# Optimization experiments

Measured on AMD Instinct MI355X. Metric: run time of the kernel, lower is better.

The kernel has to match this reference:

```python
import jax, jax.numpy as jnp
import numpy as np

ALPHA = 0.2       # leak rate
NOISE_STD = 0.05  # noise_std

B, T, I, H, O = 128, 1024, 64, 512, 10


def setup_inputs() -> dict:
    key = jax.random.key(0)
    k0, k1, k2, k3, k4 = jax.random.split(key, 5)
    inp = jax.random.normal(k0, (B, T, I), dtype=jnp.float32)
    noise = jax.random.normal(k1, (B, T, H), dtype=jnp.float32)
    # parameters, initialized as in FullRankRNN.__init__
    wi = jax.random.normal(k2, (I, H), dtype=jnp.float32)                      # wi ~ N(0,1)
    si = jnp.ones((I,), dtype=jnp.float32)                                     # input scaling
    wrec = jax.random.normal(k3, (H, H), dtype=jnp.float32) * (1.0 / np.sqrt(H))  # rho/sqrt(H), rho=1
    wo = jax.random.normal(k4, (H, O), dtype=jnp.float32) * (5.0 / H)          # std = 5/hidden
    so = jnp.ones((O,), dtype=jnp.float32)                                     # output scaling
    h0 = jnp.zeros((H,), dtype=jnp.float32)
    return {"input": inp, "noise": noise, "wi": wi, "si": si,
            "wrec": wrec, "wo": wo, "so": so, "h0": h0}


def reference(input, noise, wi, si, wrec, wo, so, h0):
    # proxy parameters: wi_full = (wi.T * si).T = wi * si[:,None]; wo_full = wo * so
    wi_full = wi * si[:, None]          # [I, H]
    wo_full = wo * so                   # [H, O] (so broadcasts over output dim)
    h_init = jnp.broadcast_to(h0, (input.shape[0], h0.shape[0]))  # [B, H]

    def step(h, xs):
        x_t, n_t = xs                   # [B, I], [B, H]
        r = jax.nn.relu(h)
        h_new = h + ALPHA * (-h + x_t @ wi_full + r @ wrec.T) + NOISE_STD * n_t
        out_t = jax.nn.relu(h_new) @ wo_full   # [B, O]
        return h_new, out_t

    xs = (jnp.swapaxes(input, 0, 1), jnp.swapaxes(noise, 0, 1))  # time-major
    _, outs = jax.lax.scan(step, h_init, xs)                     # [T, B, O]
    return jnp.swapaxes(outs, 0, 1)                              # [B, T, O]
```

## Files before the change

kernel.cpp:

```cpp
#include <hip/hip_runtime.h>

typedef _Float16 h2 __attribute__((ext_vector_type(2)));
typedef unsigned int uint;
typedef unsigned short ushort;

#define ALPHA 0.2f
#define NSTD  0.05f
#define BB 128
#define TT 1024
#define II 64
#define HH 512
#define OO 10

#define WS_NEED (512 * 12 * 16)

__device__ __forceinline__ float fdot2f(h2 a, h2 b, float c) {
#if __has_builtin(__builtin_amdgcn_fdot2)
    return __builtin_amdgcn_fdot2(a, b, c, false);
#else
    return c + (float)a.x * (float)b.x + (float)a.y * (float)b.y;
#endif
}
__device__ __forceinline__ h2 mkh2(float a, float b) { h2 v; v.x = (_Float16)a; v.y = (_Float16)b; return v; }
__device__ __forceinline__ h2 bch2(uint u) { return __builtin_bit_cast(h2, u); }
__device__ __forceinline__ uint bcu(h2 v) { return __builtin_bit_cast(uint, v); }

#define AGPR_WRITE(dst, src) asm volatile("v_accvgpr_write_b32 %0, %1" : "=a"(dst) : "v"(src))
#define AGPR_READ(dst, src)  asm volatile("v_accvgpr_read_b32 %0, %1" : "=v"(dst) : "a"(src))

template<int CTRL>
__device__ __forceinline__ float dppadd(float v) {
    int i = __builtin_bit_cast(int, v);
    int m = __builtin_amdgcn_update_dpp(0, i, CTRL, 0xF, 0xF, true);
    return v + __builtin_bit_cast(float, m);
}
__device__ __forceinline__ float red64(float v) {
    v = dppadd<0xB1>(v);
    v = dppadd<0x4E>(v);
    v = dppadd<0x124>(v);
    v = dppadd<0x128>(v);
    v = dppadd<0x142>(v);
    v = dppadd<0x143>(v);
    return v;
}

__global__ __launch_bounds__(512) void pack_kernel(
    const float* __restrict__ wrec, const float* __restrict__ wi,
    const float* __restrict__ si, uint4* __restrict__ ws)
{
    const int tid = threadIdx.x;
    const int l = tid & 63, g = tid >> 6;
    uint4* wsp = ws + tid * 12;
#pragma unroll
    for (int r = 0; r < 2; ++r) {
        uint v[8];
#pragma unroll
        for (int c = 0; c < 8; ++c) {
            const float* wr = wrec + (size_t)(c * 64 + l) * HH + g * 64 + 60 + 2 * r;
            v[c] = bcu(mkh2(wr[0], wr[1]));
        }
        wsp[r * 2 + 0] = make_uint4(v[0], v[1], v[2], v[3]);
        wsp[r * 2 + 1] = make_uint4(v[4], v[5], v[6], v[7]);
    }
#pragma unroll
    for (int r = 2; r < 6; ++r) {
        const int k0 = g * 8 + 2 * (r - 2);
        const float sa = si[k0], sb = si[k0 + 1];
        uint v[8];
#pragma unroll
        for (int c = 0; c < 8; ++c) {
            const int j = c * 64 + l;
            v[c] = bcu(mkh2(wi[(size_t)k0 * HH + j] * sa, wi[(size_t)(k0 + 1) * HH + j] * sb));
        }
        wsp[r * 2 + 0] = make_uint4(v[0], v[1], v[2], v[3]);
        wsp[r * 2 + 1] = make_uint4(v[4], v[5], v[6], v[7]);
    }
}

template<bool PACKED>
__global__ __launch_bounds__(512, 2) void rnn_kernel(
    const float* __restrict__ input, const float* __restrict__ noise,
    const float* __restrict__ wi, const float* __restrict__ si,
    const float* __restrict__ wrec, const float* __restrict__ wo,
    const float* __restrict__ so, const float* __restrict__ h0,
    const uint4* __restrict__ wsS, float* __restrict__ out)
{
    __shared__ uint4 ldsw[16 * 512];
    __shared__ float hacc_w[8][HH];
    __shared__ __align__(16) ushort r_shm[8 * 72];
    __shared__ uint  wo2m[OO * 256];
    __shared__ float opart[8][8];

    const int tid = threadIdx.x, l = tid & 63, g = tid >> 6;
    const int b = blockIdx.x;
    const int jown = g * 64 + l;

    uint wa[22][8];
#pragma unroll
    for (int c = 0; c < 8; ++c) {
        const float* wr = wrec + (size_t)(c * 64 + l) * HH + g * 64;
#pragma unroll
        for (int p = 0; p < 22; ++p) {
            uint v = bcu(mkh2(wr[2 * p], wr[2 * p + 1]));
            AGPR_WRITE(wa[p][c], v);
        }
    }
#pragma unroll
    for (int c = 0; c < 8; ++c) {
        const float* wr = wrec + (size_t)(c * 64 + l) * HH + g * 64 + 44;
        uint4 v1, v2;
        v1.x = bcu(mkh2(wr[0], wr[1]));   v1.y = bcu(mkh2(wr[2], wr[3]));
        v1.z = bcu(mkh2(wr[4], wr[5]));   v1.w = bcu(mkh2(wr[6], wr[7]));
        v2.x = bcu(mkh2(wr[8], wr[9]));   v2.y = bcu(mkh2(wr[10], wr[11]));
        v2.z = bcu(mkh2(wr[12], wr[13])); v2.w = bcu(mkh2(wr[14], wr[15]));
        ldsw[(2 * c) * 512 + tid] = v1;
        ldsw[(2 * c + 1) * 512 + tid] = v2;
    }
    float si8[8];
    if (!PACKED) {
#pragma unroll
        for (int e = 0; e < 8; ++e) si8[e] = si[g * 8 + e];
    }
    if (g < 4) {
#pragma unroll
        for (int o = 0; o < OO; ++o) {
            float sA = so[o] * (1.0f / ALPHA);
            wo2m[o * 256 + g * 64 + l] =
                bcu(mkh2(wo[(size_t)(g * 128 + l) * OO + o] * sA,
                         wo[(size_t)(g * 128 + 64 + l) * OO + o] * sA));
        }
    }
    float hreg = h0[jown];
    ((_Float16*)r_shm)[g * 72 + l] = (_Float16)(ALPHA * fmaxf(hreg, 0.f));
    if (g == 0) {
        float x0 = input[(size_t)b * TT * II + l];
        ((_Float16*)r_shm)[(l >> 3) * 72 + 64 + (l & 7)] = (_Float16)(ALPHA * x0);
    }
    __syncthreads();

    const uint4* r4 = ((const uint4*)r_shm) + g * 9;
    const uint4* wsp = wsS + tid * 12;
    int nidx = b * TT * HH + jown;
    const int ob = (g >> 2) * 5, q = g & 3;
    const int pa = (2 * q) * 72 + l, pb = pa + 72;
    float* outp = out + (size_t)b * TT * OO;

    auto out_duty = [&]() {
        h2 rr; rr.x = ((const _Float16*)r_shm)[pa]; rr.y = ((const _Float16*)r_shm)[pb];
        float op0 = fdot2f(rr, bch2(wo2m[(ob + 0) * 256 + q * 64 + l]), 0.f);
        float op1 = fdot2f(rr, bch2(wo2m[(ob + 1) * 256 + q * 64 + l]), 0.f);
        float op2 = fdot2f(rr, bch2(wo2m[(ob + 2) * 256 + q * 64 + l]), 0.f);
        float op3 = fdot2f(rr, bch2(wo2m[(ob + 3) * 256 + q * 64 + l]), 0.f);
        float op4 = fdot2f(rr, bch2(wo2m[(ob + 4) * 256 + q * 64 + l]), 0.f);
        op0 = red64(op0); op1 = red64(op1); op2 = red64(op2);
        op3 = red64(op3); op4 = red64(op4);
        if (l == 63) {
            opart[g][0] = op0; opart[g][1] = op1; opart[g][2] = op2;
            opart[g][3] = op3; opart[g][4] = op4;
        }
    };

    uint4 R0g = r4[0], R1g = r4[1];

#pragma unroll 1
    for (int t = 0; t < TT; ++t) {
        float nval = noise[nidx]; nidx += HH;
        float xnext = 0.f;
        if (g == 0 && t + 1 < TT) xnext = input[(size_t)b * TT * II + (size_t)(t + 1) * II + l];

        out_duty();

        float acc[8] = {0.f, 0.f, 0.f, 0.f, 0.f, 0.f, 0.f, 0.f};

#pragma unroll
        for (int qq = 0; qq < 5; ++qq) {
            uint4 R = (qq == 0) ? R0g : (qq == 1) ? R1g : r4[qq];
            uint rc[4] = {R.x, R.y, R.z, R.w};
#pragma unroll
            for (int pp = 0; pp < 4; ++pp) {
                const h2 rr = bch2(rc[pp]);
                const int p = 4 * qq + pp;
#pragma unroll
                for (int c = 0; c < 8; ++c) {
                    uint wv; AGPR_READ(wv, wa[p][c]);
                    acc[c] = fdot2f(bch2(wv), rr, acc[c]);
                }
            }
        }
        uint4 R5 = r4[5], R6 = r4[6], R7 = r4[7], R8 = r4[8];
        {
            const h2 r20 = bch2(R5.x), r21 = bch2(R5.y);
#pragma unroll
            for (int c = 0; c < 8; ++c) {
                uint w0, w1;
                AGPR_READ(w0, wa[20][c]); AGPR_READ(w1, wa[21][c]);
                acc[c] = fdot2f(bch2(w0), r20, acc[c]);
                acc[c] = fdot2f(bch2(w1), r21, acc[c]);
            }
        }
        {
            const h2 r22 = bch2(R5.z), r23 = bch2(R5.w);
            const h2 r24 = bch2(R6.x), r25 = bch2(R6.y), r26 = bch2(R6.z), r27 = bch2(R6.w);
            const h2 r28 = bch2(R7.x), r29 = bch2(R7.y);
#pragma unroll
            for (int c = 0; c < 8; ++c) {
                uint4 L1 = ldsw[(2 * c) * 512 + tid];
                uint4 L2 = ldsw[(2 * c + 1) * 512 + tid];
                acc[c] = fdot2f(bch2(L1.x), r22, acc[c]);
                acc[c] = fdot2f(bch2(L1.y), r23, acc[c]);
                acc[c] = fdot2f(bch2(L1.z), r24, acc[c]);
                acc[c] = fdot2f(bch2(L1.w), r25, acc[c]);
                acc[c] = fdot2f(bch2(L2.x), r26, acc[c]);
                acc[c] = fdot2f(bch2(L2.y), r27, acc[c]);
                acc[c] = fdot2f(bch2(L2.z), r28, acc[c]);
                acc[c] = fdot2f(bch2(L2.w), r29, acc[c]);
            }
        }
        {
            const h2 r30 = bch2(R7.z), r31 = bch2(R7.w);
            const h2 r32 = bch2(R8.x), r33 = bch2(R8.y), r34 = bch2(R8.z), r35 = bch2(R8.w);
            if (PACKED) {
#pragma unroll
                for (int h = 0; h < 2; ++h) {
                    uint4 S0 = wsp[0 * 2 + h], S1 = wsp[1 * 2 + h], S2 = wsp[2 * 2 + h];
                    uint4 S3 = wsp[3 * 2 + h], S4 = wsp[4 * 2 + h], S5 = wsp[5 * 2 + h];
                    uint s0[4] = {S0.x, S0.y, S0.z, S0.w}; uint s1[4] = {S1.x, S1.y, S1.z, S1.w};
                    uint s2[4] = {S2.x, S2.y, S2.z, S2.w}; uint s3[4] = {S3.x, S3.y, S3.z, S3.w};
                    uint s4[4] = {S4.x, S4.y, S4.z, S4.w}; uint s5[4] = {S5.x, S5.y, S5.z, S5.w};
#pragma unroll
                    for (int cc = 0; cc < 4; ++cc) {
                        const int c = 4 * h + cc;
                        acc[c] = fdot2f(bch2(s0[cc]), r30, acc[c]);
                        acc[c] = fdot2f(bch2(s1[cc]), r31, acc[c]);
                        acc[c] = fdot2f(bch2(s2[cc]), r32, acc[c]);
                        acc[c] = fdot2f(bch2(s3[cc]), r33, acc[c]);
                        acc[c] = fdot2f(bch2(s4[cc]), r34, acc[c]);
                        acc[c] = fdot2f(bch2(s5[cc]), r35, acc[c]);
                    }
                }
            } else {
#pragma unroll
                for (int c = 0; c < 8; ++c) {
                    const int j = c * 64 + l;
                    const float* wr = wrec + (size_t)j * HH + g * 64 + 60;
                    float4 f = *(const float4*)wr;
                    acc[c] = fdot2f(mkh2(f.x, f.y), r30, acc[c]);
                    acc[c] = fdot2f(mkh2(f.z, f.w), r31, acc[c]);
                    float a0 = wi[(size_t)(g * 8 + 0) * HH + j] * si8[0];
                    float a1 = wi[(size_t)(g * 8 + 1) * HH + j] * si8[1];
                    float a2 = wi[(size_t)(g * 8 + 2) * HH + j] * si8[2];
                    float a3 = wi[(size_t)(g * 8 + 3) * HH + j] * si8[3];
                    float a4 = wi[(size_t)(g * 8 + 4) * HH + j] * si8[4];
                    float a5 = wi[(size_t)(g * 8 + 5) * HH + j] * si8[5];
                    float a6 = wi[(size_t)(g * 8 + 6) * HH + j] * si8[6];
                    float a7 = wi[(size_t)(g * 8 + 7) * HH + j] * si8[7];
                    acc[c] = fdot2f(mkh2(a0, a1), r32, acc[c]);
                    acc[c] = fdot2f(mkh2(a2, a3), r33, acc[c]);
                    acc[c] = fdot2f(mkh2(a4, a5), r34, acc[c]);
                    acc[c] = fdot2f(mkh2(a6, a7), r35, acc[c]);
                }
            }
        }
#pragma unroll
        for (int c = 0; c < 8; ++c) hacc_w[g][c * 64 + l] = acc[c];
        __syncthreads();

        if (g == 7 && l < OO && t > 0) {
            float v;
            if (l < 5) v = opart[0][l] + opart[1][l] + opart[2][l] + opart[3][l];
            else { int o = l - 5; v = opart[4][o] + opart[5][o] + opart[6][o] + opart[7][o]; }
            outp[(size_t)(t - 1) * OO + l] = v;
        }
        {
            float s0 = hacc_w[0][jown], s1 = hacc_w[1][jown];
            float s2 = hacc_w[2][jown], s3 = hacc_w[3][jown];
            float s4 = hacc_w[4][jown], s5 = hacc_w[5][jown];
            float s6 = hacc_w[6][jown], s7 = hacc_w[7][jown];
            float s = ((s0 + s1) + (s2 + s3)) + ((s4 + s5) + (s6 + s7));
            hreg = (1.f - ALPHA) * hreg + s + NSTD * nval;
        }
        ((_Float16*)r_shm)[g * 72 + l] = (_Float16)(ALPHA * fmaxf(hreg, 0.f));
        if (g == 0) ((_Float16*)r_shm)[(l >> 3) * 72 + 64 + (l & 7)] = (_Float16)(ALPHA * xnext);
        asm volatile("" ::: "memory");
        R0g = r4[0]; R1g = r4[1];
        __syncthreads();
    }

    out_duty();
    __syncthreads();
    if (g == 7 && l < OO) {
        float v;
        if (l < 5) v = opart[0][l] + opart[1][l] + opart[2][l] + opart[3][l];
        else { int o = l - 5; v = opart[4][o] + opart[5][o] + opart[6][o] + opart[7][o]; }
        outp[(size_t)(TT - 1) * OO + l] = v;
    }
}

extern "C" void kernel_launch(void* const* d_in, const int* in_sizes, int n_in,
                              void* d_out, int out_size, void* d_ws, size_t ws_size,
                              hipStream_t stream) {
    const float* input = (const float*)d_in[0];
    const float* noise = (const float*)d_in[1];
    const float* wi    = (const float*)d_in[2];
    const float* si    = (const float*)d_in[3];
    const float* wrec  = (const float*)d_in[4];
    const float* wo    = (const float*)d_in[5];
    const float* so    = (const float*)d_in[6];
    const float* h0    = (const float*)d_in[7];
    float* out = (float*)d_out;

    if (ws_size >= (size_t)WS_NEED) {
        uint4* ws = (uint4*)d_ws;
        pack_kernel<<<dim3(1), dim3(512), 0, stream>>>(wrec, wi, si, ws);
        rnn_kernel<true><<<dim3(BB), dim3(512), 0, stream>>>(
            input, noise, wi, si, wrec, wo, so, h0, ws, out);
    } else {
        rnn_kernel<false><<<dim3(BB), dim3(512), 0, stream>>>(
            input, noise, wi, si, wrec, wo, so, h0, nullptr, out);
    }
}
```

Baseline: 3.591 ms.

## Batch 16 sequences per block and compute recurrence with MFMA

Replaces the per-sequence fdot2 recurrence with blocks that each process 16 batch rows, computing the recurrent, input and output projections with 16x16x32 f16 MFMA instructions. Most recurrent weights stay in registers as MFMA B-fragments, with the remainder in LDS. Hidden state is kept in accumulator layout, and the relu'd state is double-buffered in LDS so each step needs only one barrier. The grid shrinks to 8 blocks, trading parallelism across CUs for much less serial work per step. The separate pack kernel and workspace path are removed.

```diff
diff --git a/kernel.cpp b/kernel.cpp
--- a/kernel.cpp
+++ b/kernel.cpp
@@ -1,8 +1,8 @@
 #include <hip/hip_runtime.h>
 
-typedef _Float16 h2 __attribute__((ext_vector_type(2)));
-typedef unsigned int uint;
-typedef unsigned short ushort;
+typedef _Float16 f16;
+typedef _Float16 f16x8 __attribute__((ext_vector_type(8)));
+typedef float    f32x4 __attribute__((ext_vector_type(4)));
 
 #define ALPHA 0.2f
 #define NSTD  0.05f
@@ -12,287 +12,219 @@
 #define HH 512
 #define OO 10
 
-#define WS_NEED (512 * 12 * 16)
-
-__device__ __forceinline__ float fdot2f(h2 a, h2 b, float c) {
-#if __has_builtin(__builtin_amdgcn_fdot2)
-    return __builtin_amdgcn_fdot2(a, b, c, false);
-#else
-    return c + (float)a.x * (float)b.x + (float)a.y * (float)b.y;
-#endif
+#define MB   16
+#define NB   (BB / MB)
+#define NAG  13
+#define NLD  3
+#define RSTR 584
+
+__device__ __forceinline__ f32x4 mfma16(f16x8 a, f16x8 b, f32x4 c) {
+    return __builtin_amdgcn_mfma_f32_16x16x32_f16(a, b, c, 0, 0, 0);
 }
-__device__ __forceinline__ h2 mkh2(float a, float b) { h2 v; v.x = (_Float16)a; v.y = (_Float16)b; return v; }
-__device__ __forceinline__ h2 bch2(uint u) { return __builtin_bit_cast(h2, u); }
-__device__ __forceinline__ uint bcu(h2 v) { return __builtin_bit_cast(uint, v); }
-
-#define AGPR_WRITE(dst, src) asm volatile("v_accvgpr_write_b32 %0, %1" : "=a"(dst) : "v"(src))
-#define AGPR_READ(dst, src)  asm volatile("v_accvgpr_read_b32 %0, %1" : "=v"(dst) : "a"(src))
-
-template<int CTRL>
-__device__ __forceinline__ float dppadd(float v) {
-    int i = __builtin_bit_cast(int, v);
-    int m = __builtin_amdgcn_update_dpp(0, i, CTRL, 0xF, 0xF, true);
-    return v + __builtin_bit_cast(float, m);
-}
-__device__ __forceinline__ float red64(float v) {
-    v = dppadd<0xB1>(v);
-    v = dppadd<0x4E>(v);
-    v = dppadd<0x124>(v);
-    v = dppadd<0x128>(v);
-    v = dppadd<0x142>(v);
-    v = dppadd<0x143>(v);
-    return v;
-}
-
-__global__ __launch_bounds__(512) void pack_kernel(
-    const float* __restrict__ wrec, const float* __restrict__ wi,
-    const float* __restrict__ si, uint4* __restrict__ ws)
-{
-    const int tid = threadIdx.x;
-    const int l = tid & 63, g = tid >> 6;
-    uint4* wsp = ws + tid * 12;
-#pragma unroll
-    for (int r = 0; r < 2; ++r) {
-        uint v[8];
-#pragma unroll
-        for (int c = 0; c < 8; ++c) {
-            const float* wr = wrec + (size_t)(c * 64 + l) * HH + g * 64 + 60 + 2 * r;
-            v[c] = bcu(mkh2(wr[0], wr[1]));
-        }
-        wsp[r * 2 + 0] = make_uint4(v[0], v[1], v[2], v[3]);
-        wsp[r * 2 + 1] = make_uint4(v[4], v[5], v[6], v[7]);
-    }
-#pragma unroll
-    for (int r = 2; r < 6; ++r) {
-        const int k0 = g * 8 + 2 * (r - 2);
-        const float sa = si[k0], sb = si[k0 + 1];
-        uint v[8];
-#pragma unroll
-        for (int c = 0; c < 8; ++c) {
-            const int j = c * 64 + l;
-            v[c] = bcu(mkh2(wi[(size_t)k0 * HH + j] * sa, wi[(size_t)(k0 + 1) * HH + j] * sb));
-        }
-        wsp[r * 2 + 0] = make_uint4(v[0], v[1], v[2], v[3]);
-        wsp[r * 2 + 1] = make_uint4(v[4], v[5], v[6], v[7]);
-    }
-}
-
-template<bool PACKED>
+
 __global__ __launch_bounds__(512, 2) void rnn_kernel(
     const float* __restrict__ input, const float* __restrict__ noise,
     const float* __restrict__ wi, const float* __restrict__ si,
     const float* __restrict__ wrec, const float* __restrict__ wo,
     const float* __restrict__ so, const float* __restrict__ h0,
-    const uint4* __restrict__ wsS, float* __restrict__ out)
+    float* __restrict__ out)
 {
-    __shared__ uint4 ldsw[16 * 512];
-    __shared__ float hacc_w[8][HH];
-    __shared__ __align__(16) ushort r_shm[8 * 72];
-    __shared__ uint  wo2m[OO * 256];
-    __shared__ float opart[8][8];
+    __shared__ __align__(16) f16 r_lds[2][MB][RSTR];
+    __shared__ f16x8 wrecL[NLD][32][64];
+    __shared__ f32x4 opart[2][8][64];
 
     const int tid = threadIdx.x, l = tid & 63, g = tid >> 6;
-    const int b = blockIdx.x;
-    const int jown = g * 64 + l;
-
-    uint wa[22][8];
-#pragma unroll
-    for (int c = 0; c < 8; ++c) {
-        const float* wr = wrec + (size_t)(c * 64 + l) * HH + g * 64;
-#pragma unroll
-        for (int p = 0; p < 22; ++p) {
-            uint v = bcu(mkh2(wr[2 * p], wr[2 * p + 1]));
-            AGPR_WRITE(wa[p][c], v);
-        }
-    }
-#pragma unroll
-    for (int c = 0; c < 8; ++c) {
-        const float* wr = wrec + (size_t)(c * 64 + l) * HH + g * 64 + 44;
-        uint4 v1, v2;
-        v1.x = bcu(mkh2(wr[0], wr[1]));   v1.y = bcu(mkh2(wr[2], wr[3]));
-        v1.z = bcu(mkh2(wr[4], wr[5]));   v1.w = bcu(mkh2(wr[6], wr[7]));
-        v2.x = bcu(mkh2(wr[8], wr[9]));   v2.y = bcu(mkh2(wr[10], wr[11]));
-        v2.z = bcu(mkh2(wr[12], wr[13])); v2.w = bcu(mkh2(wr[14], wr[15]));
-        ldsw[(2 * c) * 512 + tid] = v1;
-        ldsw[(2 * c + 1) * 512 + tid] = v2;
-    }
-    float si8[8];
-    if (!PACKED) {
-#pragma unroll
-        for (int e = 0; e < 8; ++e) si8[e] = si[g * 8 + e];
-    }
-    if (g < 4) {
-#pragma unroll
-        for (int o = 0; o < OO; ++o) {
-            float sA = so[o] * (1.0f / ALPHA);
-            wo2m[o * 256 + g * 64 + l] =
-                bcu(mkh2(wo[(size_t)(g * 128 + l) * OO + o] * sA,
-                         wo[(size_t)(g * 128 + 64 + l) * OO + o] * sA));
-        }
-    }
-    float hreg = h0[jown];
-    ((_Float16*)r_shm)[g * 72 + l] = (_Float16)(ALPHA * fmaxf(hreg, 0.f));
-    if (g == 0) {
-        float x0 = input[(size_t)b * TT * II + l];
-        ((_Float16*)r_shm)[(l >> 3) * 72 + 64 + (l & 7)] = (_Float16)(ALPHA * x0);
-    }
+    const int lr = l & 15, lg = l >> 4;
+    const int b0 = blockIdx.x * MB;
+
+    f16x8 bw[NAG][4];
+    f16x8 bwi[2][4];
+    f16x8 bwo[2];
+
+#pragma unroll
+    for (int kt = 0; kt < NAG; ++kt)
+#pragma unroll
+        for (int nt = 0; nt < 4; ++nt) {
+            const float* wp = wrec + (size_t)((4*g + nt)*16 + lr)*HH + kt*32 + lg*8;
+            float4 a0 = *(const float4*)wp;
+            float4 a1 = *(const float4*)(wp + 4);
+            f16x8 v;
+            v[0]=(f16)a0.x; v[1]=(f16)a0.y; v[2]=(f16)a0.z; v[3]=(f16)a0.w;
+            v[4]=(f16)a1.x; v[5]=(f16)a1.y; v[6]=(f16)a1.z; v[7]=(f16)a1.w;
+            bw[kt][nt] = v;
+        }
+#pragma unroll
+    for (int ktL = 0; ktL < NLD; ++ktL)
+#pragma unroll
+        for (int c = 0; c < 4; ++c) {
+            const int nt = c*8 + g;
+            const float* wp = wrec + (size_t)(nt*16 + lr)*HH + (NAG + ktL)*32 + lg*8;
+            float4 a0 = *(const float4*)wp;
+            float4 a1 = *(const float4*)(wp + 4);
+            f16x8 v;
+            v[0]=(f16)a0.x; v[1]=(f16)a0.y; v[2]=(f16)a0.z; v[3]=(f16)a0.w;
+            v[4]=(f16)a1.x; v[5]=(f16)a1.y; v[6]=(f16)a1.z; v[7]=(f16)a1.w;
+            wrecL[ktL][nt][l] = v;
+        }
+#pragma unroll
+    for (int k2 = 0; k2 < 2; ++k2)
+#pragma unroll
+        for (int nt = 0; nt < 4; ++nt) {
+            const int hcol = (4*g + nt)*16 + lr;
+            f16x8 v;
+#pragma unroll
+            for (int jj = 0; jj < 8; ++jj) {
+                const int i = k2*32 + lg*8 + jj;
+                v[jj] = (f16)(wi[(size_t)i*HH + hcol] * si[i]);
+            }
+            bwi[k2][nt] = v;
+        }
+    {
+        const float s = (lr < OO) ? so[lr] * (1.0f/ALPHA) : 0.0f;
+#pragma unroll
+        for (int k2 = 0; k2 < 2; ++k2) {
+            f16x8 v;
+#pragma unroll
+            for (int jj = 0; jj < 8; ++jj) {
+                const int k = (2*g + k2)*32 + lg*8 + jj;
+                v[jj] = (f16)((lr < OO) ? wo[(size_t)k*OO + lr] * s : 0.0f);
+            }
+            bwo[k2] = v;
+        }
+    }
+
+    f32x4 hs[4];
+#pragma unroll
+    for (int nt = 0; nt < 4; ++nt) {
+        const float v = h0[(4*g + nt)*16 + lr];
+        hs[nt] = f32x4{v, v, v, v};
+    }
+
+    const float* nptr[4];
+#pragma unroll
+    for (int rr = 0; rr < 4; ++rr)
+        nptr[rr] = noise + (size_t)(b0 + 4*lg + rr)*TT*HH + 64*g + lr;
+    float nz[4][4];
+#pragma unroll
+    for (int nt = 0; nt < 4; ++nt)
+#pragma unroll
+        for (int rr = 0; rr < 4; ++rr) nz[nt][rr] = nptr[rr][nt*16];
+
+    const int bb = tid >> 5, ii = (tid & 31) * 2;
+    const float* xbase = input + (size_t)(b0 + bb)*TT*II + ii;
+    float2 xv = *(const float2*)xbase;
+
+#pragma unroll
+    for (int nt = 0; nt < 4; ++nt)
+#pragma unroll
+        for (int rr = 0; rr < 4; ++rr)
+            r_lds[0][4*lg + rr][(4*g + nt)*16 + lr] =
+                (f16)(ALPHA * fmaxf(hs[nt][rr], 0.0f));
+    r_lds[0][bb][512 + ii]     = (f16)(ALPHA * xv.x);
+    r_lds[0][bb][512 + ii + 1] = (f16)(ALPHA * xv.y);
+    const float* xq = xbase + II;
+    xv = *(const float2*)xq;  xq += II;
+
     __syncthreads();
 
-    const uint4* r4 = ((const uint4*)r_shm) + g * 9;
-    const uint4* wsp = wsS + tid * 12;
-    int nidx = b * TT * HH + jown;
-    const int ob = (g >> 2) * 5, q = g & 3;
-    const int pa = (2 * q) * 72 + l, pb = pa + 72;
-    float* outp = out + (size_t)b * TT * OO;
-
-    auto out_duty = [&]() {
-        h2 rr; rr.x = ((const _Float16*)r_shm)[pa]; rr.y = ((const _Float16*)r_shm)[pb];
-        float op0 = fdot2f(rr, bch2(wo2m[(ob + 0) * 256 + q * 64 + l]), 0.f);
-        float op1 = fdot2f(rr, bch2(wo2m[(ob + 1) * 256 + q * 64 + l]), 0.f);
-        float op2 = fdot2f(rr, bch2(wo2m[(ob + 2) * 256 + q * 64 + l]), 0.f);
-        float op3 = fdot2f(rr, bch2(wo2m[(ob + 3) * 256 + q * 64 + l]), 0.f);
-        float op4 = fdot2f(rr, bch2(wo2m[(ob + 4) * 256 + q * 64 + l]), 0.f);
-        op0 = red64(op0); op1 = red64(op1); op2 = red64(op2);
-        op3 = red64(op3); op4 = red64(op4);
-        if (l == 63) {
-            opart[g][0] = op0; opart[g][1] = op1; opart[g][2] = op2;
-            opart[g][3] = op3; opart[g][4] = op4;
-        }
-    };
-
-    uint4 R0g = r4[0], R1g = r4[1];
-
+    int cur = 0;
 #pragma unroll 1
     for (int t = 0; t < TT; ++t) {
-        float nval = noise[nidx]; nidx += HH;
-        float xnext = 0.f;
-        if (g == 0 && t + 1 < TT) xnext = input[(size_t)b * TT * II + (size_t)(t + 1) * II + l];
-
-        out_duty();
-
-        float acc[8] = {0.f, 0.f, 0.f, 0.f, 0.f, 0.f, 0.f, 0.f};
-
-#pragma unroll
-        for (int qq = 0; qq < 5; ++qq) {
-            uint4 R = (qq == 0) ? R0g : (qq == 1) ? R1g : r4[qq];
-            uint rc[4] = {R.x, R.y, R.z, R.w};
-#pragma unroll
-            for (int pp = 0; pp < 4; ++pp) {
-                const h2 rr = bch2(rc[pp]);
-                const int p = 4 * qq + pp;
-#pragma unroll
-                for (int c = 0; c < 8; ++c) {
-                    uint wv; AGPR_READ(wv, wa[p][c]);
-                    acc[c] = fdot2f(bch2(wv), rr, acc[c]);
-                }
+        const f16* rb = &r_lds[cur][0][0] + lr*RSTR + lg*8;
+
+#pragma unroll
+        for (int nt = 0; nt < 4; ++nt) {
+            f32x4 a = hs[nt];
+#pragma unroll
+            for (int rr = 0; rr < 4; ++rr)
+                a[rr] = (1.0f - ALPHA)*a[rr] + NSTD*nz[nt][rr];
+            hs[nt] = a;
+        }
+        if (t + 1 < TT) {
+#pragma unroll
+            for (int rr = 0; rr < 4; ++rr) nptr[rr] += HH;
+#pragma unroll
+            for (int nt = 0; nt < 4; ++nt)
+#pragma unroll
+                for (int rr = 0; rr < 4; ++rr) nz[nt][rr] = nptr[rr][nt*16];
+        }
+
+        {
+            const f16x8 aA = *(const f16x8*)(rb + (2*g)*32);
+            const f16x8 aB = *(const f16x8*)(rb + (2*g)*32 + 32);
+            f32x4 oacc = mfma16(aA, bwo[0], f32x4{0.f, 0.f, 0.f, 0.f});
+            oacc = mfma16(aB, bwo[1], oacc);
+            opart[cur][g][l] = oacc;
+        }
+
+#pragma unroll
+        for (int kt = 0; kt < NAG; ++kt) {
+            const f16x8 a = *(const f16x8*)(rb + kt*32);
+#pragma unroll
+            for (int nt = 0; nt < 4; ++nt)
+                hs[nt] = mfma16(a, bw[kt][nt], hs[nt]);
+        }
+#pragma unroll
+        for (int ktL = 0; ktL < NLD; ++ktL) {
+            const f16x8 a = *(const f16x8*)(rb + (NAG + ktL)*32);
+#pragma unroll
+            for (int nt = 0; nt < 4; ++nt)
+                hs[nt] = mfma16(a, wrecL[ktL][4*g + nt][l], hs[nt]);
+        }
+#pragma unroll
+        for (int k2 = 0; k2 < 2; ++k2) {
+            const f16x8 a = *(const f16x8*)(rb + (16 + k2)*32);
+#pragma unroll
+            for (int nt = 0; nt < 4; ++nt)
+                hs[nt] = mfma16(a, bwi[k2][nt], hs[nt]);
+        }
+
+        const int nxt = cur ^ 1;
+#pragma unroll
+        for (int nt = 0; nt < 4; ++nt)
+#pragma unroll
+            for (int rr = 0; rr < 4; ++rr)
+                r_lds[nxt][4*lg + rr][(4*g + nt)*16 + lr] =
+                    (f16)(ALPHA * fmaxf(hs[nt][rr], 0.0f));
+        if (t + 1 < TT) {
+            r_lds[nxt][bb][512 + ii]     = (f16)(ALPHA * xv.x);
+            r_lds[nxt][bb][512 + ii + 1] = (f16)(ALPHA * xv.y);
+            if (t + 2 < TT) { xv = *(const float2*)xq; xq += II; }
+        }
+
+        __syncthreads();
+
+        if (g == 7 && t > 0) {
+            f32x4 s = opart[cur][0][l];
+#pragma unroll
+            for (int w = 1; w < 8; ++w) s += opart[cur][w][l];
+            if (lr < OO) {
+#pragma unroll
+                for (int rr = 0; rr < 4; ++rr)
+                    out[((size_t)(b0 + 4*lg + rr)*TT + (t - 1))*OO + lr] = s[rr];
             }
         }
-        uint4 R5 = r4[5], R6 = r4[6], R7 = r4[7], R8 = r4[8];
-        {
-            const h2 r20 = bch2(R5.x), r21 = bch2(R5.y);
-#pragma unroll
-            for (int c = 0; c < 8; ++c) {
-                uint w0, w1;
-                AGPR_READ(w0, wa[20][c]); AGPR_READ(w1, wa[21][c]);
-                acc[c] = fdot2f(bch2(w0), r20, acc[c]);
-                acc[c] = fdot2f(bch2(w1), r21, acc[c]);
-            }
-        }
-        {
-            const h2 r22 = bch2(R5.z), r23 = bch2(R5.w);
-            const h2 r24 = bch2(R6.x), r25 = bch2(R6.y), r26 = bch2(R6.z), r27 = bch2(R6.w);
-            const h2 r28 = bch2(R7.x), r29 = bch2(R7.y);
-#pragma unroll
-            for (int c = 0; c < 8; ++c) {
-                uint4 L1 = ldsw[(2 * c) * 512 + tid];
-                uint4 L2 = ldsw[(2 * c + 1) * 512 + tid];
-                acc[c] = fdot2f(bch2(L1.x), r22, acc[c]);
-                acc[c] = fdot2f(bch2(L1.y), r23, acc[c]);
-                acc[c] = fdot2f(bch2(L1.z), r24, acc[c]);
-                acc[c] = fdot2f(bch2(L1.w), r25, acc[c]);
-                acc[c] = fdot2f(bch2(L2.x), r26, acc[c]);
-                acc[c] = fdot2f(bch2(L2.y), r27, acc[c]);
-                acc[c] = fdot2f(bch2(L2.z), r28, acc[c]);
-                acc[c] = fdot2f(bch2(L2.w), r29, acc[c]);
-            }
-        }
-        {
-            const h2 r30 = bch2(R7.z), r31 = bch2(R7.w);
-            const h2 r32 = bch2(R8.x), r33 = bch2(R8.y), r34 = bch2(R8.z), r35 = bch2(R8.w);
-            if (PACKED) {
-#pragma unroll
-                for (int h = 0; h < 2; ++h) {
-                    uint4 S0 = wsp[0 * 2 + h], S1 = wsp[1 * 2 + h], S2 = wsp[2 * 2 + h];
-                    uint4 S3 = wsp[3 * 2 + h], S4 = wsp[4 * 2 + h], S5 = wsp[5 * 2 + h];
-                    uint s0[4] = {S0.x, S0.y, S0.z, S0.w}; uint s1[4] = {S1.x, S1.y, S1.z, S1.w};
-                    uint s2[4] = {S2.x, S2.y, S2.z, S2.w}; uint s3[4] = {S3.x, S3.y, S3.z, S3.w};
-                    uint s4[4] = {S4.x, S4.y, S4.z, S4.w}; uint s5[4] = {S5.x, S5.y, S5.z, S5.w};
-#pragma unroll
-                    for (int cc = 0; cc < 4; ++cc) {
-                        const int c = 4 * h + cc;
-                        acc[c] = fdot2f(bch2(s0[cc]), r30, acc[c]);
-                        acc[c] = fdot2f(bch2(s1[cc]), r31, acc[c]);
-                        acc[c] = fdot2f(bch2(s2[cc]), r32, acc[c]);
-                        acc[c] = fdot2f(bch2(s3[cc]), r33, acc[c]);
-                        acc[c] = fdot2f(bch2(s4[cc]), r34, acc[c]);
-                        acc[c] = fdot2f(bch2(s5[cc]), r35, acc[c]);
-                    }
-                }
-            } else {
-#pragma unroll
-                for (int c = 0; c < 8; ++c) {
-                    const int j = c * 64 + l;
-                    const float* wr = wrec + (size_t)j * HH + g * 64 + 60;
-                    float4 f = *(const float4*)wr;
-                    acc[c] = fdot2f(mkh2(f.x, f.y), r30, acc[c]);
-                    acc[c] = fdot2f(mkh2(f.z, f.w), r31, acc[c]);
-                    float a0 = wi[(size_t)(g * 8 + 0) * HH + j] * si8[0];
-                    float a1 = wi[(size_t)(g * 8 + 1) * HH + j] * si8[1];
-                    float a2 = wi[(size_t)(g * 8 + 2) * HH + j] * si8[2];
-                    float a3 = wi[(size_t)(g * 8 + 3) * HH + j] * si8[3];
-                    float a4 = wi[(size_t)(g * 8 + 4) * HH + j] * si8[4];
-                    float a5 = wi[(size_t)(g * 8 + 5) * HH + j] * si8[5];
-                    float a6 = wi[(size_t)(g * 8 + 6) * HH + j] * si8[6];
-                    float a7 = wi[(size_t)(g * 8 + 7) * HH + j] * si8[7];
-                    acc[c] = fdot2f(mkh2(a0, a1), r32, acc[c]);
-                    acc[c] = fdot2f(mkh2(a2, a3), r33, acc[c]);
-                    acc[c] = fdot2f(mkh2(a4, a5), r34, acc[c]);
-                    acc[c] = fdot2f(mkh2(a6, a7), r35, acc[c]);
-                }
-            }
-        }
-#pragma unroll
-        for (int c = 0; c < 8; ++c) hacc_w[g][c * 64 + l] = acc[c];
-        __syncthreads();
-
-        if (g == 7 && l < OO && t > 0) {
-            float v;
-            if (l < 5) v = opart[0][l] + opart[1][l] + opart[2][l] + opart[3][l];
-            else { int o = l - 5; v = opart[4][o] + opart[5][o] + opart[6][o] + opart[7][o]; }
-            outp[(size_t)(t - 1) * OO + l] = v;
-        }
-        {
-            float s0 = hacc_w[0][jown], s1 = hacc_w[1][jown];
-            float s2 = hacc_w[2][jown], s3 = hacc_w[3][jown];
-            float s4 = hacc_w[4][jown], s5 = hacc_w[5][jown];
-            float s6 = hacc_w[6][jown], s7 = hacc_w[7][jown];
-            float s = ((s0 + s1) + (s2 + s3)) + ((s4 + s5) + (s6 + s7));
-            hreg = (1.f - ALPHA) * hreg + s + NSTD * nval;
-        }
-        ((_Float16*)r_shm)[g * 72 + l] = (_Float16)(ALPHA * fmaxf(hreg, 0.f));
-        if (g == 0) ((_Float16*)r_shm)[(l >> 3) * 72 + 64 + (l & 7)] = (_Float16)(ALPHA * xnext);
-        asm volatile("" ::: "memory");
-        R0g = r4[0]; R1g = r4[1];
-        __syncthreads();
-    }
-
-    out_duty();
+        cur = nxt;
+    }
+
+    {
+        const f16* rb = &r_lds[cur][0][0] + lr*RSTR + lg*8;
+        const f16x8 aA = *(const f16x8*)(rb + (2*g)*32);
+        const f16x8 aB = *(const f16x8*)(rb + (2*g)*32 + 32);
+        f32x4 oacc = mfma16(aA, bwo[0], f32x4{0.f, 0.f, 0.f, 0.f});
+        oacc = mfma16(aB, bwo[1], oacc);
+        opart[cur][g][l] = oacc;
+    }
     __syncthreads();
-    if (g == 7 && l < OO) {
-        float v;
-        if (l < 5) v = opart[0][l] + opart[1][l] + opart[2][l] + opart[3][l];
-        else { int o = l - 5; v = opart[4][o] + opart[5][o] + opart[6][o] + opart[7][o]; }
-        outp[(size_t)(TT - 1) * OO + l] = v;
+    if (g == 7) {
+        f32x4 s = opart[cur][0][l];
+#pragma unroll
+        for (int w = 1; w < 8; ++w) s += opart[cur][w][l];
+        if (lr < OO) {
+#pragma unroll
+            for (int rr = 0; rr < 4; ++rr)
+                out[((size_t)(b0 + 4*lg + rr)*TT + (TT - 1))*OO + lr] = s[rr];
+        }
     }
 }
 
@@ -308,14 +240,8 @@
     const float* so    = (const float*)d_in[6];
     const float* h0    = (const float*)d_in[7];
     float* out = (float*)d_out;
-
-    if (ws_size >= (size_t)WS_NEED) {
-        uint4* ws = (uint4*)d_ws;
-        pack_kernel<<<dim3(1), dim3(512), 0, stream>>>(wrec, wi, si, ws);
-        rnn_kernel<true><<<dim3(BB), dim3(512), 0, stream>>>(
-            input, noise, wi, si, wrec, wo, so, h0, ws, out);
-    } else {
-        rnn_kernel<false><<<dim3(BB), dim3(512), 0, stream>>>(
-            input, noise, wi, si, wrec, wo, so, h0, nullptr, out);
-    }
+    (void)d_ws; (void)ws_size; (void)in_sizes; (void)n_in; (void)out_size;
+
+    rnn_kernel<<<dim3(NB), dim3(512), 0, stream>>>(
+        input, noise, wi, si, wrec, wo, so, h0, out);
 }
```

New measurement: 6.709 ms. +86.8%, slower.
